# Optimization experiments

Measured on AMD Instinct MI355X. Metric: run time of the kernel, lower is better.

The kernel has to match this reference:

```python
import jax, jax.numpy as jnp
import numpy as np

OUT_H, OUT_W = 128, 2048  # output_size
B, H, W = 64, 128, 2048


def setup_inputs() -> dict:
    key = jax.random.key(0)
    k1, k2, k3 = jax.random.split(key, 3)
    x = jax.random.normal(k1, (B, H, W), dtype=jnp.float32)
    # localization net = flatten + Dense(H*W -> 6); small init + identity bias
    w_loc = jax.random.normal(k2, (H * W, 6), dtype=jnp.float32) * 1e-4
    b_loc = jnp.array([1.0, 0.0, 0.0, 0.0, 1.0, 0.0], dtype=jnp.float32) \
        + jax.random.normal(k3, (6,), dtype=jnp.float32) * 0.01
    return {"x": x, "w_loc": w_loc, "b_loc": b_loc}


def reference(x, w_loc, b_loc):
    b, h, w = x.shape
    # --- localization net: theta (B, 2, 3) ---
    theta = (x.reshape(b, h * w) @ w_loc + b_loc).reshape(b, 2, 3)

    # --- unnormalized output-pixel grid, homogeneous coords (3, N) ---
    xs = jnp.linspace(0.0, OUT_W - 1.0, OUT_W, dtype=jnp.float32)
    ys = jnp.linspace(0.0, OUT_H - 1.0, OUT_H, dtype=jnp.float32)
    xc, yc = jnp.meshgrid(xs, ys)  # (OUT_H, OUT_W)
    grid = jnp.stack([xc.ravel(), yc.ravel(), jnp.ones(OUT_H * OUT_W, jnp.float32)], 0)

    # --- affine transform: (B,2,3) @ (3,N) -> (B,2,N), input pixel coords ---
    tg = jnp.einsum('bij,jn->bin', theta, grid)
    xq, yq = tg[:, 0, :], tg[:, 1, :]  # (B, N)

    # --- clamped bilinear interpolation ---
    x0 = jnp.floor(xq).astype(jnp.int32)
    y0 = jnp.floor(yq).astype(jnp.int32)
    x0c = jnp.clip(x0, 0, w - 1)
    x1c = jnp.clip(x0 + 1, 0, w - 1)
    y0c = jnp.clip(y0, 0, h - 1)
    y1c = jnp.clip(y0 + 1, 0, h - 1)

    flat = x.reshape(b, h * w)

    def gather(yi, xi):  # (B, N) values
        return jnp.take_along_axis(flat, yi * w + xi, axis=1)

    Ia = gather(y0c, x0c)
    Ib = gather(y1c, x0c)
    Ic = gather(y0c, x1c)
    Id = gather(y1c, x1c)

    x0f, x1f = x0c.astype(jnp.float32), x1c.astype(jnp.float32)
    y0f, y1f = y0c.astype(jnp.float32), y1c.astype(jnp.float32)
    wa = (x1f - xq) * (y1f - yq)
    wb = (x1f - xq) * (yq - y0f)
    wc = (xq - x0f) * (y1f - yq)
    wd = (xq - x0f) * (yq - y0f)

    out = wa * Ia + wb * Ib + wc * Ic + wd * Id
    return out.reshape(b, OUT_H, OUT_W)
```

## Files before the change

### kernel.cpp

```cpp
#include <hip/hip_runtime.h>

#define B_   64
#define H_   128
#define W_   2048
#define HW_  (H_ * W_)
#define OH_  128
#define OW_  2048

typedef float nfloat4 __attribute__((ext_vector_type(4)));
typedef float f2v __attribute__((ext_vector_type(2), aligned(4)));

#define QBLK 320
#define NBLK 820

__device__ __forceinline__ int blk_off(int blk) {
    if (blk <= 818) return blk * QBLK;
    return 261952;
}
__device__ __forceinline__ int blk_len(int blk) {
    return (blk < 818) ? 320 : 192;
}

#define XSTR 81
__global__ __launch_bounds__(192)
void st_block_sums(const float* __restrict__ x, const float* __restrict__ w,
                   float* __restrict__ part)
{
    __shared__ float4 xs4[32 * XSTR];
    __shared__ float  wt[6 * QBLK];
    const int kblk = blockIdx.x >> 1;
    const int half = blockIdx.x & 1;
    const int tid  = threadIdx.x;

    const int off = blk_off(kblk);
    const int len = blk_len(kblk);
    const int nt4 = len >> 2;
    const int b0  = half * 32;

    const int widx = tid >> 6;
    const int lane = tid & 63;

#pragma unroll
    for (int i = 0; i < 14; ++i) {
        const int base = i * 192 + widx * 64;
        if (base < 32 * XSTR) {
            const int idx = base + lane;
            if (idx < 32 * XSTR) {
                const int r  = idx / XSTR;
                const int f4 = idx % XSTR;
                const int ug = (f4 < nt4) ? f4 : 0;
                const float* gp = x + (size_t)(b0 + r) * HW_ + off + ug * 4;
                __builtin_amdgcn_global_load_lds(
                    (const __attribute__((address_space(1))) unsigned int*)gp,
                    (__attribute__((address_space(3))) unsigned int*)&xs4[base],
                    16, 0, 0);
            }
        }
    }

    float wreg[10];
#pragma unroll
    for (int i = 0; i < 10; ++i) {
        const int e = tid + i * 192;
        wreg[i] = (e < 6 * len) ? w[(size_t)off * 6 + e] : 0.f;
    }
#pragma unroll
    for (int i = 0; i < 10; ++i) {
        const int e = tid + i * 192;
        if (e < 6 * len) wt[(e % 6) * QBLK + (e / 6)] = wreg[i];
    }
    __syncthreads();

    const int j = tid >> 5;
    const int b = tid & 31;

    const float4* __restrict__ xr = xs4 + b * XSTR;
    const float*  __restrict__ wr = wt + j * QBLK;

    float a = 0.f;
    if (nt4 == 80) {
#pragma unroll
        for (int t4 = 0; t4 < 80; ++t4) {
            const float4 xv = xr[t4];
            const float4 wv = *(const float4*)(wr + t4 * 4);
            a = fmaf(xv.x, wv.x, a);
            a = fmaf(xv.y, wv.y, a);
            a = fmaf(xv.z, wv.z, a);
            a = fmaf(xv.w, wv.w, a);
        }
    } else {
#pragma unroll
        for (int t4 = 0; t4 < 48; ++t4) {
            const float4 xv = xr[t4];
            const float4 wv = *(const float4*)(wr + t4 * 4);
            a = fmaf(xv.x, wv.x, a);
            a = fmaf(xv.y, wv.y, a);
            a = fmaf(xv.z, wv.z, a);
            a = fmaf(xv.w, wv.w, a);
        }
    }

    part[(size_t)kblk * 384 + (size_t)(b0 + b) * 6 + j] = a;
}

__global__ __launch_bounds__(64)
void st_theta_final(const float* __restrict__ part, const float* __restrict__ bl,
                    float* __restrict__ theta)
{
#pragma clang fp contract(off)
    const int i = blockIdx.x * 64 + threadIdx.x;
    const int j = i % 6;
    const float* __restrict__ p = part + i;

    float acc;
    {
        float r[64];
#pragma unroll
        for (int u = 0; u < 64; ++u) r[u] = p[(size_t)u * 384];
        acc = r[0];
#pragma unroll
        for (int u = 1; u < 64; ++u) acc = acc + r[u];
    }
    for (int base = 64; base < 768; base += 64) {
        float r[64];
#pragma unroll
        for (int u = 0; u < 64; ++u) r[u] = p[(size_t)(base + u) * 384];
#pragma unroll
        for (int u = 0; u < 64; ++u) acc = acc + r[u];
    }
    {
        float r[52];
#pragma unroll
        for (int u = 0; u < 52; ++u) r[u] = p[(size_t)(768 + u) * 384];
#pragma unroll
        for (int u = 0; u < 52; ++u) acc = acc + r[u];
    }
    theta[i] = acc + bl[j];
}

__global__ __launch_bounds__(256)
void st_sample(const float* __restrict__ x, const float* __restrict__ theta,
               float* __restrict__ out)
{
#pragma clang fp contract(off)
    __shared__ float th[6];
    const int blk = blockIdx.x;
    const int b   = blk >> 8;
    const int rem = blk & 255;
    const int yo  = rem >> 1;
    const int seg = rem & 1;

    if (threadIdx.x < 6) th[threadIdx.x] = theta[b * 6 + threadIdx.x];
    __syncthreads();

    const float t00 = th[0], t01 = th[1], t02 = th[2];
    const float t10 = th[3], t11 = th[4], t12 = th[5];

    const int xo0 = seg * 1024 + threadIdx.x * 4;
    const float* __restrict__ img = x + (size_t)b * HW_;
    const float yof = (float)yo;

    const float cx1 = t01 * yof;
    const float cy1 = t11 * yof;

    nfloat4 o;
#pragma unroll
    for (int i = 0; i < 4; ++i) {
        const float xof = (float)(xo0 + i);
        const float px  = t00 * xof;
        const float sx  = px + cx1;
        const float xq  = sx + t02;
        const float py  = t10 * xof;
        const float sy  = py + cy1;
        const float yq  = sy + t12;

        const float xf0 = floorf(xq);
        const float yf0 = floorf(yq);

        const float x0f = __builtin_amdgcn_fmed3f(xf0,        0.f, 2047.f);
        const float x1f = __builtin_amdgcn_fmed3f(xf0 + 1.0f, 0.f, 2047.f);
        const float y0f = __builtin_amdgcn_fmed3f(yf0,        0.f,  127.f);
        const float y1f = __builtin_amdgcn_fmed3f(yf0 + 1.0f, 0.f,  127.f);

        const float basef = fminf(x0f, 2046.0f);
        const int base_i = (int)basef;
        const int y0c    = (int)y0f;
        const int y1c    = (int)y1f;

        const f2v v0 = *(const f2v*)(img + y0c * W_ + base_i);
        const f2v v1 = *(const f2v*)(img + y1c * W_ + base_i);

        const bool hiA = (x0f == 2047.0f);
        const bool loC = (x1f == basef);
        const float Ia = hiA ? v0.y : v0.x;
        const float Ic = loC ? v0.x : v0.y;
        const float Ib = hiA ? v1.y : v1.x;
        const float Id = loC ? v1.x : v1.y;

        const float gx = x1f - xq;
        const float fx = xq - x0f;
        const float gy = y1f - yq;
        const float fy = yq - y0f;

        const float wa = gx * gy;
        const float wb = gx * fy;
        const float wc = fx * gy;
        const float wd = fx * fy;

        const float pa = wa * Ia;
        const float pb = wb * Ib;
        const float s1 = pa + pb;
        const float pc = wc * Ic;
        const float s2 = s1 + pc;
        const float pd = wd * Id;
        o[i] = s2 + pd;
    }

    const size_t oidx = ((size_t)b * OH_ + yo) * OW_ + xo0;
    __builtin_nontemporal_store(o, (nfloat4*)(out + oidx));
}

extern "C" void kernel_launch(void* const* d_in, const int* in_sizes, int n_in,
                              void* d_out, int out_size, void* d_ws, size_t ws_size,
                              hipStream_t stream)
{
    const float* x  = (const float*)d_in[0];
    const float* w  = (const float*)d_in[1];
    const float* bl = (const float*)d_in[2];
    float* out = (float*)d_out;

    float* part  = (float*)d_out;
    float* theta = (float*)d_ws;

    st_block_sums<<<NBLK * 2, 192, 0, stream>>>(x, w, part);
    st_theta_final<<<6, 64, 0, stream>>>(part, bl, theta);
    st_sample<<<B_ * OH_ * 2, 256, 0, stream>>>(x, theta, out);
}
```

Before: 69.21 us.

## Double-buffer block-sum staging to overlap second-half loads with first-half compute

Result: no change. 69.56 us (+0.5%).

```diff
diff --git a/kernel.cpp b/kernel.cpp
--- a/kernel.cpp
+++ b/kernel.cpp
@@ -21,86 +21,103 @@
     return (blk < 818) ? 320 : 192;
 }
 
-#define XSTR 81
+#define XS2 41
 __global__ __launch_bounds__(192)
 void st_block_sums(const float* __restrict__ x, const float* __restrict__ w,
                    float* __restrict__ part)
 {
-    __shared__ float4 xs4[32 * XSTR];
-    __shared__ float  wt[6 * QBLK];
+    __shared__ float4 xb[2][32 * XS2];
+    __shared__ float  wb[2][6 * 160];
     const int kblk = blockIdx.x >> 1;
     const int half = blockIdx.x & 1;
     const int tid  = threadIdx.x;
 
-    const int off = blk_off(kblk);
-    const int len = blk_len(kblk);
-    const int nt4 = len >> 2;
-    const int b0  = half * 32;
+    const int off  = blk_off(kblk);
+    const int len  = blk_len(kblk);
+    const int lenh = len >> 1;
+    const int nt4h = lenh >> 2;
+    const int b0   = half * 32;
 
     const int widx = tid >> 6;
     const int lane = tid & 63;
 
-#pragma unroll
-    for (int i = 0; i < 14; ++i) {
-        const int base = i * 192 + widx * 64;
-        if (base < 32 * XSTR) {
-            const int idx = base + lane;
-            if (idx < 32 * XSTR) {
-                const int r  = idx / XSTR;
-                const int f4 = idx % XSTR;
-                const int ug = (f4 < nt4) ? f4 : 0;
-                const float* gp = x + (size_t)(b0 + r) * HW_ + off + ug * 4;
-                __builtin_amdgcn_global_load_lds(
-                    (const __attribute__((address_space(1))) unsigned int*)gp,
-                    (__attribute__((address_space(3))) unsigned int*)&xs4[base],
-                    16, 0, 0);
-            }
-        }
-    }
-
-    float wreg[10];
-#pragma unroll
-    for (int i = 0; i < 10; ++i) {
-        const int e = tid + i * 192;
-        wreg[i] = (e < 6 * len) ? w[(size_t)off * 6 + e] : 0.f;
-    }
-#pragma unroll
-    for (int i = 0; i < 10; ++i) {
-        const int e = tid + i * 192;
-        if (e < 6 * len) wt[(e % 6) * QBLK + (e / 6)] = wreg[i];
-    }
+#define STAGE_X(s)                                                            \
+    _Pragma("unroll")                                                         \
+    for (int i = 0; i < 7; ++i) {                                             \
+        const int base = i * 192 + widx * 64;                                 \
+        if (base < 32 * XS2) {                                                \
+            const int idx = base + lane;                                      \
+            if (idx < 32 * XS2) {                                             \
+                const int r  = idx / XS2;                                     \
+                const int f4 = idx % XS2;                                     \
+                const int ug = (f4 < nt4h) ? f4 : 0;                          \
+                const float* gp = x + (size_t)(b0 + r) * HW_ + off            \
+                                  + (s) * lenh + ug * 4;                      \
+                __builtin_amdgcn_global_load_lds(                             \
+                    (const __attribute__((address_space(1))) unsigned int*)gp,\
+                    (__attribute__((address_space(3))) unsigned int*)&xb[s][base],\
+                    16, 0, 0);                                                \
+            }                                                                 \
+        }                                                                     \
+    }
+
+#define WLOAD(s, rg)                                                          \
+    _Pragma("unroll")                                                         \
+    for (int i = 0; i < 5; ++i) {                                             \
+        const int e = tid + i * 192;                                          \
+        rg[i] = (e < 6 * lenh) ? w[((size_t)off + (size_t)(s) * lenh) * 6 + e]\
+                               : 0.f;                                         \
+    }
+
+#define WSTORE(s, rg)                                                         \
+    _Pragma("unroll")                                                         \
+    for (int i = 0; i < 5; ++i) {                                             \
+        const int e = tid + i * 192;                                          \
+        if (e < 6 * lenh) wb[s][(e % 6) * 160 + (e / 6)] = rg[i];             \
+    }
+
+#define COMPUTE(xr, wq, N)                                                    \
+    _Pragma("unroll")                                                         \
+    for (int t4 = 0; t4 < (N); ++t4) {                                        \
+        const float4 xv = (xr)[t4];                                           \
+        const float4 wv = *(const float4*)((wq) + t4 * 4);                    \
+        a = fmaf(xv.x, wv.x, a); a = fmaf(xv.y, wv.y, a);                     \
+        a = fmaf(xv.z, wv.z, a); a = fmaf(xv.w, wv.w, a);                     \
+    }
+
+    float wr0[5], wr1[5];
+    STAGE_X(0)
+    WLOAD(0, wr0)
+    WSTORE(0, wr0)
     __syncthreads();
 
     const int j = tid >> 5;
     const int b = tid & 31;
-
-    const float4* __restrict__ xr = xs4 + b * XSTR;
-    const float*  __restrict__ wr = wt + j * QBLK;
+    const float4* __restrict__ xr0 = &xb[0][b * XS2];
+    const float4* __restrict__ xr1 = &xb[1][b * XS2];
+    const float*  __restrict__ wq0 = &wb[0][j * 160];
+    const float*  __restrict__ wq1 = &wb[1][j * 160];
 
     float a = 0.f;
-    if (nt4 == 80) {
-#pragma unroll
-        for (int t4 = 0; t4 < 80; ++t4) {
-            const float4 xv = xr[t4];
-            const float4 wv = *(const float4*)(wr + t4 * 4);
-            a = fmaf(xv.x, wv.x, a);
-            a = fmaf(xv.y, wv.y, a);
-            a = fmaf(xv.z, wv.z, a);
-            a = fmaf(xv.w, wv.w, a);
-        }
-    } else {
-#pragma unroll
-        for (int t4 = 0; t4 < 48; ++t4) {
-            const float4 xv = xr[t4];
-            const float4 wv = *(const float4*)(wr + t4 * 4);
-            a = fmaf(xv.x, wv.x, a);
-            a = fmaf(xv.y, wv.y, a);
-            a = fmaf(xv.z, wv.z, a);
-            a = fmaf(xv.w, wv.w, a);
-        }
-    }
+
+    STAGE_X(1)
+    WLOAD(1, wr1)
+
+    if (nt4h == 40) { COMPUTE(xr0, wq0, 40) }
+    else            { COMPUTE(xr0, wq0, 24) }
+
+    WSTORE(1, wr1)
+    __syncthreads();
+
+    if (nt4h == 40) { COMPUTE(xr1, wq1, 40) }
+    else            { COMPUTE(xr1, wq1, 24) }
 
     part[(size_t)kblk * 384 + (size_t)(b0 + b) * 6 + j] = a;
+
+#undef STAGE_X
+#undef WLOAD
+#undef WSTORE
+#undef COMPUTE
 }
 
 __global__ __launch_bounds__(64)
```
